# Optimization experiments

Measured on AMD Instinct MI355X. Metric: run time of the kernel, lower is better.

The kernel has to match this reference:

```python
import jax, jax.numpy as jnp
import numpy as np

GAMMA = 0.01


def softor(x, axis, gamma=GAMMA):
    # gamma * logsumexp(x/gamma) with NSFR-style normalization when max > 1
    ls = gamma * jax.nn.logsumexp(x / gamma, axis=axis)
    return ls / jnp.maximum(jnp.max(ls), 1.0)


def clause_eval(x, I, gamma=GAMMA):
    # x: [B, G] valuations; I: [C, G, S, L] int indices into G
    gathered = x[:, I]                      # [B, C, G, S, L]  (gather along G)
    body = jnp.prod(gathered, axis=-1)      # [B, C, G, S]  product over body atoms
    return softor(body, axis=-1, gamma=gamma)  # [B, C, G]  soft-OR over substitutions


def r_step(x, W, I, gamma=GAMMA):
    C = clause_eval(x, I, gamma)            # [B, C, G]
    W_star = jax.nn.softmax(W, axis=1)      # [m, C]
    H = jnp.einsum('mc,bcg->mbg', W_star, C)  # [m, B, G]
    return softor(H, axis=0, gamma=gamma)   # [B, G]


def reference(x, W, I, infer_step):
    R = x
    for _ in range(infer_step):
        R = softor(jnp.stack([R, r_step(R, W, I)], axis=1), axis=1)  # [B, G]
    return R


def setup_inputs():
    key = jax.random.key(0)
    k1, k2, k3 = jax.random.split(key, 3)
    B, G, C, S, L, m = 16, 8192, 16, 8, 3, 1
    x = jax.random.uniform(k1, (B, G), dtype=jnp.float32)
    I = jax.random.randint(k2, (C, G, S, L), 0, G, dtype=jnp.int32)
    W = jax.random.uniform(k3, (m, C), dtype=jnp.float32)
    return {"x": x, "W": W, "I": I, "infer_step": 4}
```

## Files before the change

### kernel.cpp

```cpp
#include <hip/hip_runtime.h>
#include <hip/hip_fp16.h>

constexpr int B = 16;
constexpr int G = 8192;
constexpr int C = 16;
constexpr int S = 8;
constexpr int L = 3;
constexpr int STEPS = 4;
constexpr int NSLOT = 64;
constexpr int ARR = NSLOT * 16;

#define K_E   144.269504088896f
#define GLN2  0.00693147180560f

typedef float f4 __attribute__((ext_vector_type(4)));

__device__ __forceinline__ float fexp2(float x){ return __builtin_amdgcn_exp2f(x); }
__device__ __forceinline__ float flog2(float x){ return __builtin_amdgcn_logf(x); }

__device__ __forceinline__ void atomicMaxF(float* p, float v){
    atomicMax(reinterpret_cast<unsigned int*>(p), __float_as_uint(v));
}

__device__ __forceinline__ float waveMax(float v){
    #pragma unroll
    for (int off = 32; off > 0; off >>= 1)
        v = fmaxf(v, __shfl_down(v, off));
    return v;
}

__device__ __forceinline__ float waveSlotMax(const float* __restrict__ slots){
    float v = slots[(threadIdx.x & 63) << 4];
    v = fmaxf(v, __shfl_xor(v, 32));
    v = fmaxf(v, __shfl_xor(v, 16));
    v = fmaxf(v, __shfl_xor(v, 8));
    v = fmaxf(v, __shfl_xor(v, 4));
    v = fmaxf(v, __shfl_xor(v, 2));
    v = fmaxf(v, __shfl_xor(v, 1));
    return __builtin_amdgcn_readfirstlane(v);
}

template<bool PK>
__global__ __launch_bounds__(256) void prep_kernel(
        const float* __restrict__ x, const int* __restrict__ I,
        const float* __restrict__ W,
        float* __restrict__ wstar, float* __restrict__ slots,
        ushort* __restrict__ Ipk,
        float* __restrict__ T0, __half* __restrict__ Thh0)
{
    constexpr int NPACK = PK ? (C*G*S*L/4)/256 : 0;
    const int bid = blockIdx.x;
    if (PK && bid < NPACK){
        int t = bid*256 + threadIdx.x;
        int4 v = ((const int4*)I)[t];
        ushort4 o;
        o.x = (ushort)v.x; o.y = (ushort)v.y; o.z = (ushort)v.z; o.w = (ushort)v.w;
        ((ushort4*)Ipk)[t] = o;
    } else if (bid < NPACK + (B*G)/256){
        int t = (bid - NPACK)*256 + threadIdx.x;
        int b = t >> 13;
        int g = t & (G-1);
        float v = x[t];
        T0[g*B + b] = v;
        if (PK) Thh0[((size_t)(b>>3)*G + g)*8 + (b&7)] = __float2half(v);
    } else {
        int t = threadIdx.x;
        for (int i = t; i < 13*ARR; i += 256) slots[i] = 0.f;
        if (t == 0){
            slots[12*ARR] = 1.0f;
            float mx = -1e30f;
            for (int c = 0; c < C; c++) mx = fmaxf(mx, W[c]);
            float e[C]; float s = 0.f;
            for (int c = 0; c < C; c++){ e[c] = fexp2((W[c]-mx)*1.44269504089f); s += e[c]; }
            for (int c = 0; c < C; c++) wstar[c] = e[c] / s;
        }
    }
}

__global__ __launch_bounds__(1024) void clause_lds(
        const __half*  __restrict__ Thh,
        const ushort*  __restrict__ I16,
        const float*   __restrict__ wstar,
        const float*   __restrict__ slotPrev,
        float* __restrict__ slotLs,
        float* __restrict__ slotHu,
        float* __restrict__ Hu)
{
    extern __shared__ __align__(16) unsigned sSt[];

    const int tix = threadIdx.x;
    const int bh  = blockIdx.x >> 7;
    const int g0  = (blockIdx.x & 127) * 64;

    const uint4* src = (const uint4*)(Thh + (size_t)bh*G*8);
    uint4* dst = (uint4*)sSt;
    #pragma unroll
    for (int r = 0; r < 8; r++) dst[tix + r*1024] = src[tix + r*1024];

    const float scPrev = 1.0f / fmaxf(waveSlotMax(slotPrev), 1.0f);
    const float sc3 = scPrev * scPrev * scPrev;

    __syncthreads();

    const int lane = tix & 63;
    const int wib  = tix >> 6;
    const int c    = lane >> 2;
    const int bp   = lane & 3;
    const float wc = wstar[c];
    const int gw0  = g0 + wib*4;

    float lsm = 0.f, humax = 0.f;

    #pragma unroll 2
    for (int gi = 0; gi < 4; gi++){
        const int g = gw0 + gi;
        const uint4* ip = (const uint4*)(I16 + ((size_t)c*G + g)*24);
        uint4 q0 = ip[0], q1 = ip[1], q2 = ip[2];
        unsigned dw[12] = {q0.x,q0.y,q0.z,q0.w, q1.x,q1.y,q1.z,q1.w,
                           q2.x,q2.y,q2.z,q2.w};
        unsigned hv[24];
        #pragma unroll
        for (int i = 0; i < 12; i++){
            hv[2*i]   = sSt[(dw[i] & 0xFFFFu)*4 + bp];
            hv[2*i+1] = sSt[(dw[i] >> 16)*4 + bp];
        }
        float bx[S], by[S];
        #pragma unroll
        for (int s = 0; s < S; s++){
            float2 u0 = __half22float2(*(const __half2*)&hv[3*s+0]);
            float2 u1 = __half22float2(*(const __half2*)&hv[3*s+1]);
            float2 u2 = __half22float2(*(const __half2*)&hv[3*s+2]);
            bx[s] = u0.x*u1.x*u2.x*sc3;
            by[s] = u0.y*u1.y*u2.y*sc3;
        }
        float mx = bx[0], my = by[0];
        #pragma unroll
        for (int s = 1; s < S; s++){ mx = fmaxf(mx, bx[s]); my = fmaxf(my, by[s]); }
        float sx = 0.f, sy = 0.f;
        #pragma unroll
        for (int s = 0; s < S; s++){
            sx += fexp2((bx[s]-mx)*K_E);
            sy += fexp2((by[s]-my)*K_E);
        }
        float lx = mx + GLN2*flog2(sx);
        float ly = my + GLN2*flog2(sy);
        lsm = fmaxf(lsm, fmaxf(lx, ly));

        float hx = wc*lx, hy = wc*ly;
        hx += __shfl_xor(hx, 4); hx += __shfl_xor(hx, 8);
        hx += __shfl_xor(hx, 16); hx += __shfl_xor(hx, 32);
        hy += __shfl_xor(hy, 4); hy += __shfl_xor(hy, 8);
        hy += __shfl_xor(hy, 16); hy += __shfl_xor(hy, 32);
        humax = fmaxf(humax, fmaxf(hx, hy));

        if (c == 0)
            *(float2*)(Hu + (size_t)g*B + bh*8 + bp*2) = make_float2(hx, hy);
    }

    float wl = waveMax(lsm);
    float wh = waveMax(humax);
    if (lane == 0){
        const int wv = blockIdx.x*16 + wib;
        atomicMaxF(&slotLs[(wv & (NSLOT-1)) << 4], wl);
        atomicMaxF(&slotHu[(wv & (NSLOT-1)) << 4], wh);
    }
}

__global__ __launch_bounds__(256) void clause_bh(
        const __half*  __restrict__ Thh,
        const ushort*  __restrict__ I16,
        const float*   __restrict__ wstar,
        const float*   __restrict__ slotPrev,
        float* __restrict__ slotLs,
        float* __restrict__ slotHu,
        float* __restrict__ Hu)
{
    const int lane = threadIdx.x & 63;
    const int g    = blockIdx.x*4 + (threadIdx.x >> 6);
    const int j    = lane >> 4;
    const int b    = lane & 15;
    const __half* Tb = Thh + (size_t)(b>>3)*G*8 + (b&7);

    const float scPrev = 1.0f / fmaxf(waveSlotMax(slotPrev), 1.0f);
    const float sc3 = scPrev * scPrev * scPrev;
    const f4 wst4 = *(const f4*)(wstar + j*4);

    float humix = 0.f, lsmax = 0.f;
    #pragma unroll 2
    for (int k = 0; k < 4; k++){
        const int c = j*4 + k;
        const uint4* p = (const uint4*)(I16 + (size_t)(c*G + g)*(S*L));
        uint4 d0 = p[0], d1 = p[1], d2 = p[2];
        unsigned dw[12] = {d0.x,d0.y,d0.z,d0.w, d1.x,d1.y,d1.z,d1.w,
                           d2.x,d2.y,d2.z,d2.w};
        float gv[S*L];
        #pragma unroll
        for (int i = 0; i < 12; i++){
            gv[2*i]   = __half2float(Tb[(size_t)(dw[i] & 0xFFFFu)*8]);
            gv[2*i+1] = __half2float(Tb[(size_t)(dw[i] >> 16)*8]);
        }
        float body[S];
        #pragma unroll
        for (int s = 0; s < S; s++) body[s] = gv[3*s]*gv[3*s+1]*gv[3*s+2]*sc3;

        float m = body[0];
        #pragma unroll
        for (int s = 1; s < S; s++) m = fmaxf(m, body[s]);
        float sum = 0.f;
        #pragma unroll
        for (int s = 0; s < S; s++) sum += fexp2((body[s] - m) * K_E);
        float ls = m + GLN2 * flog2(sum);

        lsmax = fmaxf(lsmax, ls);
        humix = __builtin_fmaf(wst4[k], ls, humix);
    }
    humix += __shfl_xor(humix, 16);
    humix += __shfl_xor(humix, 32);
    if (lane < 16) Hu[(size_t)g*B + lane] = humix;

    float wl = waveMax(lsmax);
    float wh = waveMax(humix);
    if (lane == 0){
        atomicMaxF(&slotLs[(g & (NSLOT-1)) << 4], wl);
        atomicMaxF(&slotHu[(g & (NSLOT-1)) << 4], wh);
    }
}

__global__ __launch_bounds__(256) void clause_f(
        const float* __restrict__ Tin,
        const int*   __restrict__ I32,
        const float* __restrict__ wstar,
        const float* __restrict__ slotPrev,
        float* __restrict__ slotLs,
        float* __restrict__ slotHu,
        float* __restrict__ Hu)
{
    const int lane = threadIdx.x & 63;
    const int g    = blockIdx.x*4 + (threadIdx.x >> 6);
    const int j    = lane >> 4;
    const int b    = lane & 15;

    const float scPrev = 1.0f / fmaxf(waveSlotMax(slotPrev), 1.0f);
    const float sc3 = scPrev * scPrev * scPrev;
    const f4 wst4 = *(const f4*)(wstar + j*4);

    float humix = 0.f, lsmax = 0.f;
    #pragma unroll 2
    for (int k = 0; k < 4; k++){
        const int c = j*4 + k;
        const int4* p = (const int4*)(I32 + (size_t)(c*G + g)*(S*L));
        int idx[S*L];
        #pragma unroll
        for (int i = 0; i < 6; i++){
            int4 v = p[i];
            idx[4*i] = v.x; idx[4*i+1] = v.y; idx[4*i+2] = v.z; idx[4*i+3] = v.w;
        }
        float gv[S*L];
        #pragma unroll
        for (int t = 0; t < S*L; t++) gv[t] = Tin[idx[t]*B + b];

        float body[S];
        #pragma unroll
        for (int s = 0; s < S; s++) body[s] = gv[3*s]*gv[3*s+1]*gv[3*s+2]*sc3;

        float m = body[0];
        #pragma unroll
        for (int s = 1; s < S; s++) m = fmaxf(m, body[s]);
        float sum = 0.f;
        #pragma unroll
        for (int s = 0; s < S; s++) sum += fexp2((body[s] - m) * K_E);
        float ls = m + GLN2 * flog2(sum);

        lsmax = fmaxf(lsmax, ls);
        humix = __builtin_fmaf(wst4[k], ls, humix);
    }
    humix += __shfl_xor(humix, 16);
    humix += __shfl_xor(humix, 32);
    if (lane < 16) Hu[(size_t)g*B + lane] = humix;

    float wl = waveMax(lsmax);
    float wh = waveMax(humix);
    if (lane == 0){
        atomicMaxF(&slotLs[(g & (NSLOT-1)) << 4], wl);
        atomicMaxF(&slotHu[(g & (NSLOT-1)) << 4], wh);
    }
}

template<bool PK>
__global__ __launch_bounds__(256) void combine_kernel(
        const float* __restrict__ Hu,
        const float* __restrict__ Tin,
        const float* __restrict__ slotLs,
        const float* __restrict__ slotHu,
        const float* __restrict__ slotPrev,
        float* __restrict__ Tout,
        __half* __restrict__ Touth,
        float* __restrict__ slotT)
{
    const float scA = 1.0f / fmaxf(waveSlotMax(slotLs), 1.0f);
    const float scB = 1.0f / fmaxf(scA * waveSlotMax(slotHu), 1.0f);
    const float scP = 1.0f / fmaxf(waveSlotMax(slotPrev), 1.0f);

    const int t = blockIdx.x*256 + threadIdx.x;
    float r  = Hu[t] * (scA * scB);
    float Rn = Tin[t] * scP;
    float M  = fmaxf(Rn, r);
    float v  = M + GLN2 * flog2(fexp2((Rn-M)*K_E) + fexp2((r-M)*K_E));
    Tout[t] = v;
    if (PK){
        int g = t >> 4, b = t & 15;
        Touth[((size_t)(b>>3)*G + g)*8 + (b&7)] = __float2half(v);
    }
    float wm = waveMax(v);
    if ((threadIdx.x & 63) == 0)
        atomicMaxF(&slotT[(blockIdx.x & (NSLOT-1)) << 4], wm);
}

__global__ void output_kernel(const float* __restrict__ T, const float* __restrict__ slotT,
                              float* __restrict__ out){
    float sc = 1.0f / fmaxf(waveSlotMax(slotT), 1.0f);
    int tid = blockIdx.x*256 + threadIdx.x;
    int b = tid >> 13;
    int g = tid & (G-1);
    out[tid] = T[g*B + b] * sc;
}

extern "C" void kernel_launch(void* const* d_in, const int* in_sizes, int n_in,
                              void* d_out, int out_size, void* d_ws, size_t ws_size,
                              hipStream_t stream) {
    const float* x = (const float*)d_in[0];
    const float* W = (const float*)d_in[1];
    const int*   I = (const int*)d_in[2];

    const size_t baseF  = 16 + 13*ARR;
    const size_t packF  = (size_t)C*G*S*L / 2;
    const size_t stateF = (size_t)G*B;
    const size_t halfF  = (size_t)G*B / 2;
    const bool packed = ws_size >= (baseF + packF + 3*stateF + 2*halfF) * sizeof(float);

    float* ws    = (float*)d_ws;
    float* wstar = ws;
    float* slots = ws + 16;
    ushort* Ipk  = (ushort*)(ws + baseF);
    float* T0    = ws + baseF + (packed ? packF : 0);
    float* T1    = T0 + stateF;
    float* Hu    = T1 + stateF;
    __half* Thh0 = (__half*)(Hu + stateF);
    __half* Thh1 = Thh0 + (size_t)G*B;

    float* out = (float*)d_out;

    bool ldsOK = false;
    if (packed)
        ldsOK = hipFuncSetAttribute((const void*)clause_lds,
                    hipFuncAttributeMaxDynamicSharedMemorySize, 131072) == hipSuccess;

    if (packed){
        prep_kernel<true><<<(C*G*S*L/4)/256 + (B*G)/256 + 1, 256, 0, stream>>>(
            x, I, W, wstar, slots, Ipk, T0, Thh0);
    } else {
        prep_kernel<false><<<(B*G)/256 + 1, 256, 0, stream>>>(
            x, I, W, wstar, slots, Ipk, T0, Thh0);
    }

    float*  bufs[2]  = {T0, T1};
    __half* bufsh[2] = {Thh0, Thh1};
    for (int s = 0; s < STEPS; s++){
        float*  Tin   = bufs[s & 1];
        float*  Tout  = bufs[(s+1) & 1];
        __half* Tinh  = bufsh[s & 1];
        __half* Touth = bufsh[(s+1) & 1];
        float* slotLs = slots + (s*3 + 0)*ARR;
        float* slotHu = slots + (s*3 + 1)*ARR;
        float* slotT  = slots + (s*3 + 2)*ARR;
        const float* slotPrev = (s == 0) ? (slots + 12*ARR) : (slots + ((s-1)*3 + 2)*ARR);
        if (packed){
            if (ldsOK)
                clause_lds<<<256, 1024, 131072, stream>>>(Tinh, Ipk, wstar, slotPrev,
                                                          slotLs, slotHu, Hu);
            else
                clause_bh<<<G/4, 256, 0, stream>>>(Tinh, Ipk, wstar, slotPrev,
                                                   slotLs, slotHu, Hu);
            combine_kernel<true><<<(G*B)/256, 256, 0, stream>>>(Hu, Tin, slotLs, slotHu,
                                                                slotPrev, Tout, Touth, slotT);
        } else {
            clause_f<<<G/4, 256, 0, stream>>>(Tin, I, wstar, slotPrev,
                                              slotLs, slotHu, Hu);
            combine_kernel<false><<<(G*B)/256, 256, 0, stream>>>(Hu, Tin, slotLs, slotHu,
                                                                 slotPrev, Tout, Touth, slotT);
        }
    }
    output_kernel<<<(B*G)/256, 256, 0, stream>>>(bufs[STEPS & 1],
                                                 slots + ((STEPS-1)*3 + 2)*ARR, out);
}
```

Measured before the change: 78.02 us.

## Remap clause_lds lanes so each thread gathers full 16-byte LDS rows

Changes the lane mapping in clause_lds. Previously each lane handled one clause and one batch pair, and looped over 4 g values using scalar 4-byte LDS reads. Now each lane handles one clause and one g, and reads a full uint4 (8 batches of halfs) per index. This cuts the index global loads per lane, the LDS instruction count and the per-g shuffle reductions. The trade-off is higher register pressure (64 body floats) and possibly more LDS bank conflicts from the wide random reads.

```diff
diff --git a/kernel.cpp b/kernel.cpp
--- a/kernel.cpp
+++ b/kernel.cpp
@@ -86,16 +86,15 @@
         float* __restrict__ slotHu,
         float* __restrict__ Hu)
 {
-    extern __shared__ __align__(16) unsigned sSt[];
+    extern __shared__ __align__(16) uint4 sSt4[];
 
     const int tix = threadIdx.x;
     const int bh  = blockIdx.x >> 7;
     const int g0  = (blockIdx.x & 127) * 64;
 
     const uint4* src = (const uint4*)(Thh + (size_t)bh*G*8);
-    uint4* dst = (uint4*)sSt;
-    #pragma unroll
-    for (int r = 0; r < 8; r++) dst[tix + r*1024] = src[tix + r*1024];
+    #pragma unroll
+    for (int r = 0; r < 8; r++) sSt4[tix + r*1024] = src[tix + r*1024];
 
     const float scPrev = 1.0f / fmaxf(waveSlotMax(slotPrev), 1.0f);
     const float sc3 = scPrev * scPrev * scPrev;
@@ -104,57 +103,69 @@
 
     const int lane = tix & 63;
     const int wib  = tix >> 6;
-    const int c    = lane >> 2;
-    const int bp   = lane & 3;
+    const int c    = lane & 15;
+    const int gsub = lane >> 4;
+    const int g    = g0 + wib*4 + gsub;
     const float wc = wstar[c];
-    const int gw0  = g0 + wib*4;
-
-    float lsm = 0.f, humax = 0.f;
-
-    #pragma unroll 2
-    for (int gi = 0; gi < 4; gi++){
-        const int g = gw0 + gi;
-        const uint4* ip = (const uint4*)(I16 + ((size_t)c*G + g)*24);
-        uint4 q0 = ip[0], q1 = ip[1], q2 = ip[2];
-        unsigned dw[12] = {q0.x,q0.y,q0.z,q0.w, q1.x,q1.y,q1.z,q1.w,
-                           q2.x,q2.y,q2.z,q2.w};
-        unsigned hv[24];
-        #pragma unroll
-        for (int i = 0; i < 12; i++){
-            hv[2*i]   = sSt[(dw[i] & 0xFFFFu)*4 + bp];
-            hv[2*i+1] = sSt[(dw[i] >> 16)*4 + bp];
+
+    const uint4* ip = (const uint4*)(I16 + ((size_t)c*G + g)*24);
+    uint4 q0 = ip[0], q1 = ip[1], q2 = ip[2];
+    unsigned dw[12] = {q0.x,q0.y,q0.z,q0.w, q1.x,q1.y,q1.z,q1.w,
+                       q2.x,q2.y,q2.z,q2.w};
+    int ix[24];
+    #pragma unroll
+    for (int i = 0; i < 12; i++){
+        ix[2*i]   = (int)(dw[i] & 0xFFFFu);
+        ix[2*i+1] = (int)(dw[i] >> 16);
+    }
+
+    float body[S][8];
+    #pragma unroll
+    for (int s = 0; s < S; s++){
+        uint4 r0 = sSt4[ix[3*s+0]];
+        uint4 r1 = sSt4[ix[3*s+1]];
+        uint4 r2 = sSt4[ix[3*s+2]];
+        #pragma unroll
+        for (int h = 0; h < 4; h++){
+            float2 a  = __half22float2(((const __half2*)&r0)[h]);
+            float2 b2 = __half22float2(((const __half2*)&r1)[h]);
+            float2 c2 = __half22float2(((const __half2*)&r2)[h]);
+            body[s][2*h]   = a.x*b2.x*c2.x*sc3;
+            body[s][2*h+1] = a.y*b2.y*c2.y*sc3;
         }
-        float bx[S], by[S];
-        #pragma unroll
-        for (int s = 0; s < S; s++){
-            float2 u0 = __half22float2(*(const __half2*)&hv[3*s+0]);
-            float2 u1 = __half22float2(*(const __half2*)&hv[3*s+1]);
-            float2 u2 = __half22float2(*(const __half2*)&hv[3*s+2]);
-            bx[s] = u0.x*u1.x*u2.x*sc3;
-            by[s] = u0.y*u1.y*u2.y*sc3;
-        }
-        float mx = bx[0], my = by[0];
-        #pragma unroll
-        for (int s = 1; s < S; s++){ mx = fmaxf(mx, bx[s]); my = fmaxf(my, by[s]); }
-        float sx = 0.f, sy = 0.f;
-        #pragma unroll
-        for (int s = 0; s < S; s++){
-            sx += fexp2((bx[s]-mx)*K_E);
-            sy += fexp2((by[s]-my)*K_E);
-        }
-        float lx = mx + GLN2*flog2(sx);
-        float ly = my + GLN2*flog2(sy);
-        lsm = fmaxf(lsm, fmaxf(lx, ly));
-
-        float hx = wc*lx, hy = wc*ly;
-        hx += __shfl_xor(hx, 4); hx += __shfl_xor(hx, 8);
-        hx += __shfl_xor(hx, 16); hx += __shfl_xor(hx, 32);
-        hy += __shfl_xor(hy, 4); hy += __shfl_xor(hy, 8);
-        hy += __shfl_xor(hy, 16); hy += __shfl_xor(hy, 32);
-        humax = fmaxf(humax, fmaxf(hx, hy));
-
-        if (c == 0)
-            *(float2*)(Hu + (size_t)g*B + bh*8 + bp*2) = make_float2(hx, hy);
+    }
+
+    float hu[8];
+    float lsm = 0.f;
+    #pragma unroll
+    for (int bl = 0; bl < 8; bl++){
+        float m = body[0][bl];
+        #pragma unroll
+        for (int s = 1; s < S; s++) m = fmaxf(m, body[s][bl]);
+        float sum = 0.f;
+        #pragma unroll
+        for (int s = 0; s < S; s++) sum += fexp2((body[s][bl] - m) * K_E);
+        float ls = m + GLN2 * flog2(sum);
+        lsm = fmaxf(lsm, ls);
+        hu[bl] = wc * ls;
+    }
+
+    #pragma unroll
+    for (int bl = 0; bl < 8; bl++){
+        hu[bl] += __shfl_xor(hu[bl], 1);
+        hu[bl] += __shfl_xor(hu[bl], 2);
+        hu[bl] += __shfl_xor(hu[bl], 4);
+        hu[bl] += __shfl_xor(hu[bl], 8);
+    }
+    float humax = hu[0];
+    #pragma unroll
+    for (int bl = 1; bl < 8; bl++) humax = fmaxf(humax, hu[bl]);
+
+    if (c == 0){
+        f4 v0 = {hu[0], hu[1], hu[2], hu[3]};
+        f4 v1 = {hu[4], hu[5], hu[6], hu[7]};
+        *(f4*)(Hu + (size_t)g*B + bh*8)     = v0;
+        *(f4*)(Hu + (size_t)g*B + bh*8 + 4) = v1;
     }
 
     float wl = waveMax(lsm);
```

New measurement: 71.93 us. 7.8% less time.
